# Kernel optimization log

Measured on AMD Instinct MI355X. Metric: run time of the kernel, lower is better.

## Reference

```python
import jax, jax.numpy as jnp
import numpy as np

N_NODES = 100_000   # number of nodes
N_EDGES = 1_600_000 # number of edges (avg degree 16)
D_IN    = 64        # node feature dim
E_W     = 16        # edge feature ('w') dim -> message dim D_IN + E_W
EPS     = 0.0       # init_eps, non-learnable buffer


def setup_inputs() -> dict:
    key = jax.random.key(0)
    k1, k2, k3, k4, k5 = jax.random.split(key, 5)
    feat = jax.random.normal(k1, (N_NODES, D_IN), dtype=jnp.float32)
    edge_w = jax.random.normal(k2, (N_EDGES, E_W), dtype=jnp.float32)
    src = jax.random.randint(k3, (N_EDGES,), 0, N_NODES)
    dst = jax.random.randint(k4, (N_EDGES,), 0, N_NODES)
    # apply_func: Linear(D_IN + E_W -> D_IN)
    W = jax.random.normal(k5, (D_IN + E_W, D_IN), dtype=jnp.float32) / np.float32(np.sqrt(D_IN + E_W))
    b = jnp.zeros((D_IN,), dtype=jnp.float32)
    return {"feat": feat, "edge_w": edge_w, "W": W, "b": b, "src": src, "dst": dst}


def reference(feat, edge_w, W, b, src, dst):
    n = feat.shape[0]
    # message m_e = concat(h[src_e], w_e); sum-aggregate over incoming edges of dst.
    # Sum of concat == concat of sums, avoiding materializing [E, D_IN+E_W].
    neigh_h = jax.ops.segment_sum(feat[src], dst, num_segments=n)     # [N, D_IN]
    neigh_w = jax.ops.segment_sum(edge_w, dst, num_segments=n)        # [N, E_W]
    neigh = jnp.concatenate([neigh_h, neigh_w], axis=-1)              # [N, D_IN+E_W]
    # pad feat with zeros to match widened message dim (as in the torch code)
    feat_pad = jnp.concatenate(
        [feat, jnp.zeros((n, neigh.shape[-1] - feat.shape[-1]), feat.dtype)], axis=-1
    )
    rst = (1.0 + EPS) * feat_pad + neigh                              # eps-residual
    rst = rst @ W + b                                                 # apply_func (Linear)
    return jax.nn.relu(rst)                                           # activation
```

## Files before the change

kernel.cpp:

```cpp
#include <hip/hip_runtime.h>

#define D_IN  64
#define E_W   16
#define D_MSG 80

static __device__ __forceinline__ void f4add(float4& a, const float4& b) {
    a.x += b.x; a.y += b.y; a.z += b.z; a.w += b.w;
}

__global__ __launch_bounds__(256) void k_hist(const int* __restrict__ dst,
                                              int* __restrict__ deg, int E)
{
    int i = (blockIdx.x * 256 + threadIdx.x) * 4;
    if (i + 3 < E) {
        int4 d = *(const int4*)(dst + i);
        atomicAdd(deg + d.x, 1);
        atomicAdd(deg + d.y, 1);
        atomicAdd(deg + d.z, 1);
        atomicAdd(deg + d.w, 1);
    } else {
        for (; i < E; ++i) atomicAdd(deg + dst[i], 1);
    }
}

__global__ __launch_bounds__(256) void k_scan1(const int* __restrict__ deg,
                                               int* __restrict__ excl,
                                               int* __restrict__ bsums, int n)
{
    __shared__ int ts[256];
    int base = blockIdx.x * 1024 + threadIdx.x * 4;
    int v[4], s = 0;
    #pragma unroll
    for (int i = 0; i < 4; ++i) { v[i] = (base + i < n) ? deg[base + i] : 0; s += v[i]; }
    ts[threadIdx.x] = s; __syncthreads();
    #pragma unroll
    for (int off = 1; off < 256; off <<= 1) {
        int t = (threadIdx.x >= off) ? ts[threadIdx.x - off] : 0;
        __syncthreads();
        ts[threadIdx.x] += t;
        __syncthreads();
    }
    int run = ts[threadIdx.x] - s;
    if (threadIdx.x == 255) bsums[blockIdx.x] = ts[255];
    #pragma unroll
    for (int i = 0; i < 4; ++i) {
        if (base + i < n) excl[base + i] = run;
        run += v[i];
    }
}

__global__ __launch_bounds__(256) void k_scan2(int* __restrict__ bsums,
                                               int* __restrict__ bexcl, int nb)
{
    __shared__ int ts[256];
    int v = (threadIdx.x < nb) ? bsums[threadIdx.x] : 0;
    ts[threadIdx.x] = v; __syncthreads();
    #pragma unroll
    for (int off = 1; off < 256; off <<= 1) {
        int t = (threadIdx.x >= off) ? ts[threadIdx.x - off] : 0;
        __syncthreads();
        ts[threadIdx.x] += t;
        __syncthreads();
    }
    bexcl[threadIdx.x] = ts[threadIdx.x] - v;
}

__global__ __launch_bounds__(256) void k_scan3(const int* __restrict__ excl,
                                               const int* __restrict__ bexcl,
                                               int* __restrict__ offsets,
                                               int* __restrict__ cursor, int n, int E)
{
    int i = blockIdx.x * 256 + threadIdx.x;
    if (i < n) {
        int s = excl[i] + bexcl[i >> 10];
        offsets[i] = s;
        cursor[i]  = s;
    }
    if (i == 0) offsets[n] = E;
}

__global__ __launch_bounds__(256) void k_reorder(const int* __restrict__ src,
                                                 const int* __restrict__ dst,
                                                 int* __restrict__ cursor,
                                                 int2* __restrict__ sorted, int E)
{
    int e = blockIdx.x * 256 + threadIdx.x;
    if (e >= E) return;
    int d = dst[e];
    int pos = atomicAdd(cursor + d, 1);
    sorted[pos] = make_int2(src[e], e);
}

__global__ __launch_bounds__(256) void k_pull(const float4* __restrict__ feat4,
                                              const float4* __restrict__ ew4,
                                              const int2* __restrict__ sorted,
                                              const int* __restrict__ offsets,
                                              float4* __restrict__ acc_h4,
                                              float4* __restrict__ acc_w4, int N)
{
    int t = blockIdx.x * 256 + threadIdx.x;
    int node = t >> 4;
    if (node >= N) return;
    int l = t & 15;

    int beg = offsets[node];
    int end = offsets[node + 1];

    float4 ah = feat4[(size_t)node * 16 + l];
    float4 aw = make_float4(0.f, 0.f, 0.f, 0.f);

    if (beg < end) {
        int2 r0 = sorted[beg];
        int2 r1 = (beg + 1 < end) ? sorted[beg + 1] : make_int2(0, 0);
        for (int p = beg; p < end; ++p) {
            int2 rn = (p + 2 < end) ? sorted[p + 2] : make_int2(0, 0);
            float4 h0 = feat4[(size_t)r0.x * 16 + l];
            f4add(ah, h0);
            if (l < 4) {
                float4 w0 = ew4[(size_t)r0.y * 4 + l];
                f4add(aw, w0);
            }
            r0 = r1; r1 = rn;
        }
    }

    acc_h4[(size_t)node * 16 + l] = ah;
    if (l < 4) acc_w4[(size_t)node * 4 + l] = aw;
}

__global__ __launch_bounds__(256) void scatter_kernel(
    const float4* __restrict__ feat4, const float4* __restrict__ ew4,
    const int* __restrict__ src, const int* __restrict__ dst,
    float* __restrict__ acc_h, float* __restrict__ acc_w, int E)
{
    int t = blockIdx.x * 256 + threadIdx.x;
    int e = t >> 4;
    if (e >= E) return;
    int l = t & 15;
    int s = src[e];
    int d = dst[e];
    float4 hv = feat4[(size_t)s * 16 + l];
    float4 wv;
    bool do_w = (l < 4);
    if (do_w) wv = ew4[(size_t)e * 4 + l];
    float* p = acc_h + (size_t)d * D_IN + l * 4;
    unsafeAtomicAdd(p + 0, hv.x);
    unsafeAtomicAdd(p + 1, hv.y);
    unsafeAtomicAdd(p + 2, hv.z);
    unsafeAtomicAdd(p + 3, hv.w);
    if (do_w) {
        float* q = acc_w + (size_t)d * E_W + l * 4;
        unsafeAtomicAdd(q + 0, wv.x);
        unsafeAtomicAdd(q + 1, wv.y);
        unsafeAtomicAdd(q + 2, wv.z);
        unsafeAtomicAdd(q + 3, wv.w);
    }
}

__global__ __launch_bounds__(256) void gemm_relu_kernel(
    const float* __restrict__ feat, const float* __restrict__ acc_w,
    const float* __restrict__ Wm, const float* __restrict__ bias,
    float* __restrict__ out, int N, int add_feat)
{
    __shared__ float4 Wl[D_MSG * 16];
    __shared__ float4 bl4[16];
    __shared__ float  xs[64 * 84];

    for (int i = threadIdx.x; i < D_MSG * 16; i += 256)
        Wl[i] = ((const float4*)Wm)[i];
    if (threadIdx.x < 16)
        bl4[threadIdx.x] = ((const float4*)bias)[threadIdx.x];

    const int tc   = threadIdx.x & 15;
    const int tg   = threadIdx.x >> 4;
    const int base = blockIdx.x * 64;

    for (int i = threadIdx.x; i < 64 * 20; i += 256) {
        int r = i / 20, c = i % 20;
        int row = base + r;
        float4 v = make_float4(0.f, 0.f, 0.f, 0.f);
        if (row < N) {
            if (c < 16) {
                v = ((const float4*)out)[(size_t)row * 16 + c];
                if (add_feat) {
                    float4 f = ((const float4*)feat)[(size_t)row * 16 + c];
                    f4add(v, f);
                }
            } else {
                v = ((const float4*)acc_w)[(size_t)row * 4 + (c - 16)];
            }
        }
        *((float4*)&xs[r * 84 + c * 4]) = v;
    }
    __syncthreads();

    float4 ob = bl4[tc];
    float4 acc[4];
    acc[0] = ob; acc[1] = ob; acc[2] = ob; acc[3] = ob;

    #pragma unroll 4
    for (int k = 0; k < D_MSG; ++k) {
        float4 w = Wl[k * 16 + tc];
        #pragma unroll
        for (int rr = 0; rr < 4; ++rr) {
            float xk = xs[(tg * 4 + rr) * 84 + k];
            acc[rr].x += xk * w.x;
            acc[rr].y += xk * w.y;
            acc[rr].z += xk * w.z;
            acc[rr].w += xk * w.w;
        }
    }

    #pragma unroll
    for (int rr = 0; rr < 4; ++rr) {
        int row = base + tg * 4 + rr;
        if (row < N) {
            float4 v = acc[rr];
            v.x = fmaxf(v.x, 0.f);
            v.y = fmaxf(v.y, 0.f);
            v.z = fmaxf(v.z, 0.f);
            v.w = fmaxf(v.w, 0.f);
            ((float4*)out)[(size_t)row * 16 + tc] = v;
        }
    }
}

static inline size_t align256(size_t x) { return (x + 255) & ~(size_t)255; }

extern "C" void kernel_launch(void* const* d_in, const int* in_sizes, int n_in,
                              void* d_out, int out_size, void* d_ws, size_t ws_size,
                              hipStream_t stream) {
    const float* feat   = (const float*)d_in[0];
    const float* edge_w = (const float*)d_in[1];
    const float* Wm     = (const float*)d_in[2];
    const float* bias   = (const float*)d_in[3];
    const int*   src    = (const int*)d_in[4];
    const int*   dst    = (const int*)d_in[5];
    float* out = (float*)d_out;

    const int N = in_sizes[0] / D_IN;
    const int E = in_sizes[4];

    size_t o_accw   = 0;
    size_t o_deg    = align256(o_accw + (size_t)N * E_W * 4);
    size_t o_excl   = align256(o_deg  + (size_t)(N + 1) * 4);
    size_t o_off    = align256(o_excl + (size_t)N * 4);
    size_t o_cur    = align256(o_off  + (size_t)(N + 1) * 4);
    size_t o_bsum   = align256(o_cur  + (size_t)N * 4);
    size_t o_bexcl  = align256(o_bsum + 256 * 4);
    size_t o_sorted = align256(o_bexcl + 256 * 4);
    size_t need     = o_sorted + (size_t)E * 8;

    char* ws = (char*)d_ws;
    float* acc_w = (float*)(ws + o_accw);

    int used_fallback = 0;

    if (ws_size >= need) {
        int*  deg     = (int*) (ws + o_deg);
        int*  excl    = (int*) (ws + o_excl);
        int*  offsets = (int*) (ws + o_off);
        int*  cursor  = (int*) (ws + o_cur);
        int*  bsums   = (int*) (ws + o_bsum);
        int*  bexcl   = (int*) (ws + o_bexcl);
        int2* sorted  = (int2*)(ws + o_sorted);

        hipMemsetAsync(deg, 0, (size_t)(N + 1) * 4, stream);

        int hb = (E / 4 + 255) / 256 + 1;
        k_hist<<<hb, 256, 0, stream>>>(dst, deg, E);

        int nb1 = (N + 1023) / 1024;
        k_scan1<<<nb1, 256, 0, stream>>>(deg, excl, bsums, N);
        k_scan2<<<1, 256, 0, stream>>>(bsums, bexcl, nb1);
        k_scan3<<<(N + 255) / 256, 256, 0, stream>>>(excl, bexcl, offsets, cursor, N, E);

        k_reorder<<<(E + 255) / 256, 256, 0, stream>>>(src, dst, cursor, sorted, E);

        k_pull<<<(N * 16 + 255) / 256, 256, 0, stream>>>(
            (const float4*)feat, (const float4*)edge_w, sorted, offsets,
            (float4*)out, (float4*)acc_w, N);
    } else {
        used_fallback = 1;
        hipMemsetAsync(d_out, 0, (size_t)N * D_IN * sizeof(float), stream);
        hipMemsetAsync(acc_w, 0, (size_t)N * E_W * sizeof(float), stream);
        long long tot = (long long)E * 16;
        scatter_kernel<<<(int)((tot + 255) / 256), 256, 0, stream>>>(
            (const float4*)feat, (const float4*)edge_w, src, dst, out, acc_w, E);
    }

    gemm_relu_kernel<<<(N + 63) / 64, 256, 0, stream>>>(
        feat, acc_w, Wm, bias, out, N, used_fallback);
}
```

Before: 471.0 us.

## Shard histogram and reorder atomics by destination range across XCDs

```diff
diff --git a/kernel.cpp b/kernel.cpp
--- a/kernel.cpp
+++ b/kernel.cpp
@@ -3,23 +3,36 @@
 #define D_IN  64
 #define E_W   16
 #define D_MSG 80
+#define NXCD  8
 
 static __device__ __forceinline__ void f4add(float4& a, const float4& b) {
     a.x += b.x; a.y += b.y; a.z += b.z; a.w += b.w;
 }
 
-__global__ __launch_bounds__(256) void k_hist(const int* __restrict__ dst,
-                                              int* __restrict__ deg, int E)
-{
-    int i = (blockIdx.x * 256 + threadIdx.x) * 4;
-    if (i + 3 < E) {
-        int4 d = *(const int4*)(dst + i);
-        atomicAdd(deg + d.x, 1);
-        atomicAdd(deg + d.y, 1);
-        atomicAdd(deg + d.z, 1);
-        atomicAdd(deg + d.w, 1);
-    } else {
-        for (; i < E; ++i) atomicAdd(deg + dst[i], 1);
+__global__ __launch_bounds__(256) void k_hist_sh(const int4* __restrict__ dst4,
+                                                 const int* __restrict__ dst,
+                                                 int* __restrict__ deg,
+                                                 int E, int rng)
+{
+    int shard = blockIdx.x & (NXCD - 1);
+    int wg    = blockIdx.x / NXCD;
+    int lo    = shard * rng;
+    int hi    = lo + rng;
+    int E4    = E >> 2;
+
+    int base = wg * 512;
+    int stop = min(base + 512, E4);
+    for (int i = base + threadIdx.x; i < stop; i += 256) {
+        int4 d = dst4[i];
+        if (d.x >= lo && d.x < hi) atomicAdd(deg + d.x, 1);
+        if (d.y >= lo && d.y < hi) atomicAdd(deg + d.y, 1);
+        if (d.z >= lo && d.z < hi) atomicAdd(deg + d.z, 1);
+        if (d.w >= lo && d.w < hi) atomicAdd(deg + d.w, 1);
+    }
+    if (wg == 0 && threadIdx.x < (E & 3)) {
+        int e = (E & ~3) + threadIdx.x;
+        int d = dst[e];
+        if (d >= lo && d < hi) atomicAdd(deg + d, 1);
     }
 }
 
@@ -79,16 +92,39 @@
     if (i == 0) offsets[n] = E;
 }
 
-__global__ __launch_bounds__(256) void k_reorder(const int* __restrict__ src,
-                                                 const int* __restrict__ dst,
-                                                 int* __restrict__ cursor,
-                                                 int2* __restrict__ sorted, int E)
-{
-    int e = blockIdx.x * 256 + threadIdx.x;
-    if (e >= E) return;
-    int d = dst[e];
-    int pos = atomicAdd(cursor + d, 1);
-    sorted[pos] = make_int2(src[e], e);
+__global__ __launch_bounds__(256) void k_reorder_sh(const int4* __restrict__ src4,
+                                                    const int4* __restrict__ dst4,
+                                                    const int* __restrict__ src,
+                                                    const int* __restrict__ dst,
+                                                    int* __restrict__ cursor,
+                                                    int2* __restrict__ sorted,
+                                                    int E, int rng)
+{
+    int shard = blockIdx.x & (NXCD - 1);
+    int wg    = blockIdx.x / NXCD;
+    int lo    = shard * rng;
+    int hi    = lo + rng;
+    int E4    = E >> 2;
+
+    int base = wg * 512;
+    int stop = min(base + 512, E4);
+    for (int i = base + threadIdx.x; i < stop; i += 256) {
+        int4 d = dst4[i];
+        bool any = (d.x >= lo && d.x < hi) | (d.y >= lo && d.y < hi) |
+                   (d.z >= lo && d.z < hi) | (d.w >= lo && d.w < hi);
+        if (!any) continue;
+        int4 s = src4[i];
+        int e = i * 4;
+        if (d.x >= lo && d.x < hi) sorted[atomicAdd(cursor + d.x, 1)] = make_int2(s.x, e + 0);
+        if (d.y >= lo && d.y < hi) sorted[atomicAdd(cursor + d.y, 1)] = make_int2(s.y, e + 1);
+        if (d.z >= lo && d.z < hi) sorted[atomicAdd(cursor + d.z, 1)] = make_int2(s.z, e + 2);
+        if (d.w >= lo && d.w < hi) sorted[atomicAdd(cursor + d.w, 1)] = make_int2(s.w, e + 3);
+    }
+    if (wg == 0 && threadIdx.x < (E & 3)) {
+        int e = (E & ~3) + threadIdx.x;
+        int d = dst[e];
+        if (d >= lo && d < hi) sorted[atomicAdd(cursor + d, 1)] = make_int2(src[e], e);
+    }
 }
 
 __global__ __launch_bounds__(256) void k_pull(const float4* __restrict__ feat4,
@@ -267,15 +303,21 @@
 
         hipMemsetAsync(deg, 0, (size_t)(N + 1) * 4, stream);
 
-        int hb = (E / 4 + 255) / 256 + 1;
-        k_hist<<<hb, 256, 0, stream>>>(dst, deg, E);
+        const int rng = (N + NXCD - 1) / NXCD;
+        const int E4  = E >> 2;
+        const int wg_per_shard = (E4 + 511) / 512;
+        const int grid_sh = wg_per_shard * NXCD;
+
+        k_hist_sh<<<grid_sh, 256, 0, stream>>>(
+            (const int4*)dst, dst, deg, E, rng);
 
         int nb1 = (N + 1023) / 1024;
         k_scan1<<<nb1, 256, 0, stream>>>(deg, excl, bsums, N);
         k_scan2<<<1, 256, 0, stream>>>(bsums, bexcl, nb1);
         k_scan3<<<(N + 255) / 256, 256, 0, stream>>>(excl, bexcl, offsets, cursor, N, E);
 
-        k_reorder<<<(E + 255) / 256, 256, 0, stream>>>(src, dst, cursor, sorted, E);
+        k_reorder_sh<<<grid_sh, 256, 0, stream>>>(
+            (const int4*)src, (const int4*)dst, src, dst, cursor, sorted, E, rng);
 
         k_pull<<<(N * 16 + 255) / 256, 256, 0, stream>>>(
             (const float4*)feat, (const float4*)edge_w, sorted, offsets,
```

After: 419.8 us. -10.9%, faster.
